# Kernel optimization log

Hardware: AMD Instinct MI355X
Metric: run time of the kernel (lower is better)

## Reference

```python
import math
import jax, jax.numpy as jnp
import numpy as np

NUM_HEADS = 8
K_CRITICAL = 0.05
K_SKIP = 0.10


def setup_inputs() -> dict:
    key = jax.random.key(0)
    ks = jax.random.split(key, 10)
    B, T, D = 1, 2048, 512
    s = 1.0 / math.sqrt(D)
    return {
        'x': jax.random.normal(ks[0], (B, T, D), jnp.float32),
        'wq': jax.random.normal(ks[1], (D, D), jnp.float32) * s,
        'bq': jax.random.normal(ks[2], (D,), jnp.float32) * s,
        'wk': jax.random.normal(ks[3], (D, D), jnp.float32) * s,
        'bk': jax.random.normal(ks[4], (D,), jnp.float32) * s,
        'wv': jax.random.normal(ks[5], (D, D), jnp.float32) * s,
        'bv': jax.random.normal(ks[6], (D,), jnp.float32) * s,
        'wo': jax.random.normal(ks[7], (D, D), jnp.float32) * s,
        'bo': jax.random.normal(ks[8], (D,), jnp.float32) * s,
    }


def _phi(t):
    # elu(t) + 1 -> positive feature map for linear attention
    return jax.nn.elu(t) + 1.0


def reference(x, wq, bq, wk, bk, wv, bv, wo, bo):
    B, T, D = x.shape
    H = NUM_HEADS
    hd = D // H

    # projections (torch nn.Linear: y = x @ W.T + b), split heads -> [B,H,T,hd]
    q = (x @ wq.T + bq).reshape(B, T, H, hd).transpose(0, 2, 1, 3)
    k = (x @ wk.T + bk).reshape(B, T, H, hd).transpose(0, 2, 1, 3)
    v = (x @ wv.T + bv).reshape(B, T, H, hd).transpose(0, 2, 1, 3)

    # full attention scores [B,H,T,T]
    scores = jnp.einsum('bhqd,bhkd->bhqk', q, k) / math.sqrt(hd)

    # per-query quantile thresholds (linear interpolation, like torch.quantile)
    crit_th = jnp.quantile(scores, 1.0 - K_CRITICAL, axis=-1, keepdims=True)
    skip_th = jnp.quantile(scores, K_SKIP, axis=-1, keepdims=True)
    crit_mask = scores > crit_th
    skip_mask = scores < skip_th
    marginal_mask = jnp.logical_not(crit_mask | skip_mask)

    # critical path: softmax over top-k_critical entries only
    crit_scores = jnp.where(crit_mask, scores, -jnp.inf)
    crit_attn = jax.nn.softmax(crit_scores, axis=-1)
    crit_attn = jnp.where(skip_mask, 0.0, crit_attn)
    crit_out = jnp.einsum('bhqk,bhkd->bhqd', crit_attn, v)

    # marginal path: causal (cumulative) linear attention
    q_f = _phi(q)
    k_f = _phi(k)
    kv_cum = jnp.cumsum(k_f[..., :, None] * v[..., None, :], axis=2)  # [B,H,T,hd,hd]
    k_cum = jnp.cumsum(k_f, axis=2)                                   # [B,H,T,hd]
    lin_num = jnp.einsum('bhtd,bhtde->bhte', q_f, kv_cum)             # [B,H,T,hd]
    lin_den = jnp.clip(jnp.sum(q_f * k_cum, axis=-1, keepdims=True), 1e-6, None)
    marginal_active = jnp.mean(marginal_mask.astype(scores.dtype), axis=-1, keepdims=True)
    lin_out = (lin_num / lin_den) * marginal_active

    out = (crit_out + lin_out).transpose(0, 2, 1, 3).reshape(B, T, D)
    out = out @ wo.T + bo  # dropout is identity in eval mode
    return out
```

## Files before the change

### kernel.cpp

```cpp
#include <hip/hip_runtime.h>
#include <math.h>

#define T_SEQ 2048
#define D_MODEL 512
#define H_HEADS 8
#define HD 64
#define NCH 32
#define CSZ 64
#define CAP 192

__device__ __forceinline__ unsigned f2k(float f) {
    unsigned u = __float_as_uint(f);
    return (u & 0x80000000u) ? ~u : (u | 0x80000000u);
}
__device__ __forceinline__ float k2f(unsigned k) {
    unsigned u = (k & 0x80000000u) ? (k & 0x7fffffffu) : ~k;
    return __uint_as_float(u);
}

__device__ __forceinline__ void locate_rank(unsigned rr, unsigned e0,
    const unsigned cc[4], int lane, unsigned& sel_bin, unsigned& sel_nb, unsigned& sel_cnt)
{
    unsigned e1 = e0 + cc[0], e2 = e1 + cc[1], e3 = e2 + cc[2];
    int bin = -1; unsigned nb = 0u, ct = 0u;
    if (rr >= e0 && rr < e1)              { bin = lane * 4 + 0; nb = e0; ct = cc[0]; }
    else if (rr >= e1 && rr < e2)         { bin = lane * 4 + 1; nb = e1; ct = cc[1]; }
    else if (rr >= e2 && rr < e3)         { bin = lane * 4 + 2; nb = e2; ct = cc[2]; }
    else if (rr >= e3 && rr < e3 + cc[3]) { bin = lane * 4 + 3; nb = e3; ct = cc[3]; }
    unsigned long long bal = __ballot(bin >= 0);
    int src = __ffsll((unsigned long long)bal) - 1;
    sel_bin = (unsigned)__shfl(bin, src);
    sel_nb  = (unsigned)__shfl((int)nb, src);
    sel_cnt = (unsigned)__shfl((int)ct, src);
}

__global__ __launch_bounds__(256) void proj_qkv_kernel(
    const float* __restrict__ x,
    const float* __restrict__ wq, const float* __restrict__ bq,
    const float* __restrict__ wk, const float* __restrict__ bk,
    const float* __restrict__ wv, const float* __restrict__ bv,
    float* __restrict__ qh, float* __restrict__ kh, float* __restrict__ vh,
    float* __restrict__ qf, float* __restrict__ kf)
{
    const int which = blockIdx.z;
    const float* W    = (which == 0) ? wq : (which == 1) ? wk : wv;
    const float* bias = (which == 0) ? bq : (which == 1) ? bk : bv;
    float* outh = (which == 0) ? qh : (which == 1) ? kh : vh;
    float* outf = (which == 0) ? qf : (which == 1) ? kf : nullptr;

    __shared__ float As[32][68];
    __shared__ float Bs[32][68];
    const int tid = threadIdx.x;
    const int m0 = blockIdx.x * 64;
    const int n0 = blockIdx.y * 64;
    const int rb = (tid >> 4) * 4;
    const int cb = (tid & 15) * 4;

    float acc[4][4] = {};
    for (int k0 = 0; k0 < D_MODEL; k0 += 32) {
        for (int l = 0; l < 2; ++l) {
            int p = tid + l * 256;
            int row = p >> 3;
            int c4 = (p & 7) * 4;
            float4 av = *(const float4*)(x + (size_t)(m0 + row) * D_MODEL + k0 + c4);
            As[c4 + 0][row] = av.x; As[c4 + 1][row] = av.y;
            As[c4 + 2][row] = av.z; As[c4 + 3][row] = av.w;
            float4 wv4 = *(const float4*)(W + (size_t)(n0 + row) * D_MODEL + k0 + c4);
            Bs[c4 + 0][row] = wv4.x; Bs[c4 + 1][row] = wv4.y;
            Bs[c4 + 2][row] = wv4.z; Bs[c4 + 3][row] = wv4.w;
        }
        __syncthreads();
        #pragma unroll
        for (int kk = 0; kk < 32; ++kk) {
            float4 ar = *(const float4*)&As[kk][rb];
            float4 br = *(const float4*)&Bs[kk][cb];
            float arr[4] = {ar.x, ar.y, ar.z, ar.w};
            float brr[4] = {br.x, br.y, br.z, br.w};
            #pragma unroll
            for (int i = 0; i < 4; ++i)
                #pragma unroll
                for (int j = 0; j < 4; ++j)
                    acc[i][j] = fmaf(arr[i], brr[j], acc[i][j]);
        }
        __syncthreads();
    }
    #pragma unroll
    for (int i = 0; i < 4; ++i) {
        int m = m0 + rb + i;
        #pragma unroll
        for (int j = 0; j < 4; ++j) {
            int n = n0 + cb + j;
            float v = acc[i][j] + bias[n];
            int h = n >> 6, d = n & 63;
            size_t idx = ((size_t)(h * T_SEQ) + m) * HD + d;
            outh[idx] = v;
            if (outf) outf[idx] = (v > 0.f) ? (v + 1.f) : __expf(v);
        }
    }
}

__global__ __launch_bounds__(256) void out_proj_kernel(
    const float* __restrict__ att, const float* __restrict__ wo,
    const float* __restrict__ bo, float* __restrict__ out)
{
    __shared__ float As[32][68];
    __shared__ float Bs[32][68];
    const int tid = threadIdx.x;
    const int m0 = blockIdx.x * 64;
    const int n0 = blockIdx.y * 64;
    const int rb = (tid >> 4) * 4;
    const int cb = (tid & 15) * 4;

    float acc[4][4] = {};
    for (int k0 = 0; k0 < D_MODEL; k0 += 32) {
        for (int l = 0; l < 2; ++l) {
            int p = tid + l * 256;
            int row = p >> 3;
            int c4 = (p & 7) * 4;
            float4 av = *(const float4*)(att + (size_t)(m0 + row) * D_MODEL + k0 + c4);
            As[c4 + 0][row] = av.x; As[c4 + 1][row] = av.y;
            As[c4 + 2][row] = av.z; As[c4 + 3][row] = av.w;
            float4 wv4 = *(const float4*)(wo + (size_t)(n0 + row) * D_MODEL + k0 + c4);
            Bs[c4 + 0][row] = wv4.x; Bs[c4 + 1][row] = wv4.y;
            Bs[c4 + 2][row] = wv4.z; Bs[c4 + 3][row] = wv4.w;
        }
        __syncthreads();
        #pragma unroll
        for (int kk = 0; kk < 32; ++kk) {
            float4 ar = *(const float4*)&As[kk][rb];
            float4 br = *(const float4*)&Bs[kk][cb];
            float arr[4] = {ar.x, ar.y, ar.z, ar.w};
            float brr[4] = {br.x, br.y, br.z, br.w};
            #pragma unroll
            for (int i = 0; i < 4; ++i)
                #pragma unroll
                for (int j = 0; j < 4; ++j)
                    acc[i][j] = fmaf(arr[i], brr[j], acc[i][j]);
        }
        __syncthreads();
    }
    #pragma unroll
    for (int i = 0; i < 4; ++i) {
        int m = m0 + rb + i;
        #pragma unroll
        for (int j = 0; j < 4; ++j) {
            int n = n0 + cb + j;
            out[(size_t)m * D_MODEL + n] = acc[i][j] + bo[n];
        }
    }
}

__global__ __launch_bounds__(256) void qk_gemm_kernel(
    const float* __restrict__ qh, const float* __restrict__ kh, float* __restrict__ S)
{
    __shared__ float As[64][132];
    __shared__ float Bs[64][68];
    const int tid = threadIdx.x;
    const int n0 = blockIdx.x * 64;
    const int m0 = blockIdx.y * 128;
    const int h  = blockIdx.z;
    const float* qb = qh + (size_t)h * T_SEQ * HD;
    const float* kb = kh + (size_t)h * T_SEQ * HD;

    #pragma unroll
    for (int l = 0; l < 8; ++l) {
        int p = tid + l * 256;
        int row = p >> 4, c4 = (p & 15) * 4;
        float4 a = *(const float4*)(qb + (size_t)(m0 + row) * HD + c4);
        As[c4 + 0][row] = a.x; As[c4 + 1][row] = a.y;
        As[c4 + 2][row] = a.z; As[c4 + 3][row] = a.w;
    }
    #pragma unroll
    for (int l = 0; l < 4; ++l) {
        int p = tid + l * 256;
        int row = p >> 4, c4 = (p & 15) * 4;
        float4 b = *(const float4*)(kb + (size_t)(n0 + row) * HD + c4);
        Bs[c4 + 0][row] = b.x; Bs[c4 + 1][row] = b.y;
        Bs[c4 + 2][row] = b.z; Bs[c4 + 3][row] = b.w;
    }
    __syncthreads();

    const int rb = (tid >> 4) * 8;
    const int cb = (tid & 15) * 4;
    float acc[8][4] = {};
    #pragma unroll 8
    for (int kk = 0; kk < HD; ++kk) {
        float4 a0 = *(const float4*)&As[kk][rb];
        float4 a1 = *(const float4*)&As[kk][rb + 4];
        float4 br = *(const float4*)&Bs[kk][cb];
        float arr[8] = {a0.x, a0.y, a0.z, a0.w, a1.x, a1.y, a1.z, a1.w};
        float brr[4] = {br.x, br.y, br.z, br.w};
        #pragma unroll
        for (int i = 0; i < 8; ++i)
            #pragma unroll
            for (int j = 0; j < 4; ++j)
                acc[i][j] = fmaf(arr[i], brr[j], acc[i][j]);
    }
    #pragma unroll
    for (int i = 0; i < 8; ++i) {
        float4 o;
        o.x = acc[i][0] * 0.125f; o.y = acc[i][1] * 0.125f;
        o.z = acc[i][2] * 0.125f; o.w = acc[i][3] * 0.125f;
        *(float4*)(S + ((size_t)h * T_SEQ + m0 + rb + i) * T_SEQ + n0 + cb) = o;
    }
}

__global__ __launch_bounds__(64, 8) void select_kernel(
    const float* __restrict__ S, const float* __restrict__ vh,
    float* __restrict__ att, float* __restrict__ marg)
{
    const int h = blockIdx.y;
    const int lane = threadIdx.x;
    const int t = blockIdx.x;
    __shared__ unsigned hists[2][256];

    const float* srow = S + ((size_t)h * T_SEQ + t) * T_SEQ;
    unsigned kr[32];
    unsigned mx = 0u;
    #pragma unroll
    for (int u = 0; u < 8; ++u) {
        float4 f = *(const float4*)(srow + (size_t)(lane + u * 64) * 4);
        kr[u * 4 + 0] = f2k(f.x); kr[u * 4 + 1] = f2k(f.y);
        kr[u * 4 + 2] = f2k(f.z); kr[u * 4 + 3] = f2k(f.w);
        mx = max(mx, max(max(kr[u * 4 + 0], kr[u * 4 + 1]), max(kr[u * 4 + 2], kr[u * 4 + 3])));
    }
    #pragma unroll
    for (int off = 32; off > 0; off >>= 1)
        mx = max(mx, (unsigned)__shfl_xor(mx, off));

    unsigned pfx0, pfx1, base0 = 0u, base1 = 0u, fct0 = 0u;
    bool res0 = false, res1 = false;
    unsigned rsh1 = 0u;

    {
        uint4 z4 = make_uint4(0u, 0u, 0u, 0u);
        uint4* hv = (uint4*)hists;
        hv[lane * 2 + 0] = z4; hv[lane * 2 + 1] = z4;
        #pragma unroll
        for (int u = 0; u < 32; ++u)
            atomicAdd(&hists[0][kr[u] >> 24], 1u);
        uint4 a = ((const uint4*)hists[0])[lane];
        unsigned cc[4] = {a.x, a.y, a.z, a.w};
        unsigned lsum = cc[0] + cc[1] + cc[2] + cc[3];
        unsigned incl = lsum;
        #pragma unroll
        for (int off = 1; off < 64; off <<= 1) {
            unsigned tv = __shfl_up(incl, off);
            if (lane >= off) incl += tv;
        }
        unsigned e0 = incl - lsum;
        unsigned bin, nb, ct;
        locate_rank(204u, e0, cc, lane, bin, nb, ct);
        pfx0 = bin; base0 = nb; fct0 = ct;
        if (ct == 1u) res0 = true;
        locate_rank(1944u, e0, cc, lane, bin, nb, ct);
        pfx1 = bin; base1 = nb;
        if (ct == 1u) { res1 = true; rsh1 = 24u; }
    }

    for (int p = 1; p < 4; ++p) {
        if (res0 && res1) break;
        const int sh = 24 - 8 * p;
        const bool a0 = !res0, a1 = !res1;
        const bool dup = a0 && a1 && (pfx0 == pfx1);
        uint4 z4 = make_uint4(0u, 0u, 0u, 0u);
        uint4* hv = (uint4*)hists;
        hv[lane * 2 + 0] = z4; hv[lane * 2 + 1] = z4;
        #pragma unroll
        for (int u = 0; u < 32; ++u) {
            unsigned k = kr[u];
            unsigned hi = k >> (sh + 8);
            unsigned bin = (k >> sh) & 255u;
            if (a0 && hi == pfx0) atomicAdd(&hists[0][bin], 1u);
            if (a1 && !dup && hi == pfx1) atomicAdd(&hists[1][bin], 1u);
        }
        unsigned cc0[4], e00 = 0u;
        if (a0 || dup) {
            uint4 a = ((const uint4*)hists[0])[lane];
            cc0[0] = a.x; cc0[1] = a.y; cc0[2] = a.z; cc0[3] = a.w;
            unsigned lsum = cc0[0] + cc0[1] + cc0[2] + cc0[3];
            unsigned incl = lsum;
            #pragma unroll
            for (int off = 1; off < 64; off <<= 1) {
                unsigned tv = __shfl_up(incl, off);
                if (lane >= off) incl += tv;
            }
            e00 = incl - lsum;
        }
        if (a0) {
            unsigned bin, nb, ct;
            locate_rank(204u - base0, e00, cc0, lane, bin, nb, ct);
            pfx0 = (pfx0 << 8) | bin; base0 += nb; fct0 = ct;
            if (ct == 1u && p < 3) res0 = true;
        }
        if (a1) {
            unsigned bin, nb, ct;
            if (dup) {
                locate_rank(1944u - base1, e00, cc0, lane, bin, nb, ct);
            } else {
                uint4 b = ((const uint4*)hists[1])[lane];
                unsigned cc1[4] = {b.x, b.y, b.z, b.w};
                unsigned lsum = cc1[0] + cc1[1] + cc1[2] + cc1[3];
                unsigned incl = lsum;
                #pragma unroll
                for (int off = 1; off < 64; off <<= 1) {
                    unsigned tv = __shfl_up(incl, off);
                    if (lane >= off) incl += tv;
                }
                unsigned e10 = incl - lsum;
                locate_rank(1944u - base1, e10, cc1, lane, bin, nb, ct);
            }
            pfx1 = (pfx1 << 8) | bin; base1 += nb;
            if (ct == 1u && p < 3) { res1 = true; rsh1 = (unsigned)sh; }
        }
    }

    const unsigned cle0 = base0 + fct0;
    const unsigned scnt = (cle0 > 205u) ? base0 : cle0;
    const float m = k2f(mx);

    float2* list = (float2*)hists;
    float z = 0.f;
    unsigned bcnt = 0;
    const unsigned long long pm = (lane == 0) ? 0ull : (~0ull >> (64 - lane));
    #pragma unroll
    for (int u8 = 0; u8 < 8; ++u8) {
        #pragma unroll
        for (int q = 0; q < 4; ++q) {
            unsigned k = kr[u8 * 4 + q];
            bool crit = (k >> rsh1) > pfx1;
            unsigned long long bal = __ballot(crit);
            if (crit) {
                float sv = k2f(k);
                float w = __expf(sv - m);
                z += w;
                unsigned pos = bcnt + (unsigned)__popcll(bal & pm);
                if (pos < CAP) {
                    unsigned j = (unsigned)(4 * lane + 256 * u8 + q);
                    list[pos] = make_float2(w, __uint_as_float(j));
                }
            }
            bcnt += (unsigned)__popcll(bal);
        }
    }
    #pragma unroll
    for (int off = 32; off > 0; off >>= 1)
        z += __shfl_xor(z, off);
    const float invz = (z > 0.f) ? (1.f / z) : 0.f;

    const float* vbl = vh + (size_t)h * T_SEQ * HD + lane;
    const int cnt = (int)min(bcnt, (unsigned)CAP);
    float av[8];
    #pragma unroll
    for (int q = 0; q < 8; ++q) av[q] = 0.f;
    int i = 0;
    for (; i + 8 <= cnt; i += 8) {
        float2 e[8];
        #pragma unroll
        for (int q = 0; q < 8; ++q) e[q] = list[i + q];
        float vv[8];
        #pragma unroll
        for (int q = 0; q < 8; ++q)
            vv[q] = vbl[(size_t)__float_as_uint(e[q].y) * HD];
        #pragma unroll
        for (int q = 0; q < 8; ++q)
            av[q] = fmaf(e[q].x, vv[q], av[q]);
    }
    for (; i < cnt; ++i) {
        float2 e = list[i];
        av[0] = fmaf(e.x, vbl[(size_t)__float_as_uint(e.y) * HD], av[0]);
    }
    float acc = ((av[0] + av[1]) + (av[2] + av[3])) + ((av[4] + av[5]) + (av[6] + av[7]));
    att[(size_t)t * D_MODEL + h * HD + lane] = acc * invz;
    if (lane == 0) {
        unsigned mc = (unsigned)T_SEQ - bcnt - scnt;
        marg[(size_t)h * T_SEQ + t] = (float)mc * (1.f / (float)T_SEQ);
    }
}

__global__ __launch_bounds__(256) void chunk_sums_kernel(
    const float* __restrict__ kf, const float* __restrict__ vh,
    float* __restrict__ Ac, float* __restrict__ bc)
{
    const int c = blockIdx.x, h = blockIdx.y;
    const int tid = threadIdx.x;
    __shared__ float kfl[CSZ][HD];
    __shared__ float vl[CSZ][HD];
    const size_t base = ((size_t)h * T_SEQ + c * CSZ) * HD;

    for (int l = 0; l < 4; ++l) {
        int p = tid + l * 256;
        int row = p >> 4, c4 = (p & 15) * 4;
        *(float4*)&kfl[row][c4] = *(const float4*)(kf + base + (size_t)row * HD + c4);
        *(float4*)&vl[row][c4]  = *(const float4*)(vh + base + (size_t)row * HD + c4);
    }
    __syncthreads();

    const int d = tid >> 2, e0 = (tid & 3) * 16;
    float acc[16] = {};
    for (int u = 0; u < CSZ; ++u) {
        float a = kfl[u][d];
        #pragma unroll
        for (int i = 0; i < 16; ++i) acc[i] = fmaf(a, vl[u][e0 + i], acc[i]);
    }
    float* Adst = Ac + (((size_t)(h * NCH + c) * HD + d) * HD + e0);
    #pragma unroll
    for (int i = 0; i < 16; ++i) Adst[i] = acc[i];

    if (tid < HD) {
        float sum = 0.f;
        for (int u = 0; u < CSZ; ++u) sum += kfl[u][tid];
        bc[(size_t)(h * NCH + c) * HD + tid] = sum;
    }
}

__global__ __launch_bounds__(256) void lin_combine_kernel(
    const float* __restrict__ qf, const float* __restrict__ kf, const float* __restrict__ vh,
    const float* __restrict__ Ac, const float* __restrict__ bc,
    const float* __restrict__ marg, float* __restrict__ att)
{
    const int c = blockIdx.x, h = blockIdx.y;
    const int tid = threadIdx.x;
    __shared__ float Qs[CSZ][65];
    __shared__ float Ks[CSZ][65];
    __shared__ float P[CSZ][66];
    __shared__ float svv[HD];
    __shared__ float coef[CSZ];

    const size_t base = ((size_t)h * T_SEQ + c * CSZ) * HD;
    for (int l = 0; l < 4; ++l) {
        int p = tid + l * 256;
        int row = p >> 4, c4 = (p & 15) * 4;
        *(float4*)&Qs[row][c4] = *(const float4*)(qf + base + (size_t)row * HD + c4);
        *(float4*)&Ks[row][c4] = *(const float4*)(kf + base + (size_t)row * HD + c4);
    }

    float4 sA[4];
    #pragma unroll
    for (int l = 0; l < 4; ++l) sA[l] = make_float4(0.f, 0.f, 0.f, 0.f);
    float sb = 0.f;
    {
        const float* Abase = Ac + (size_t)(h * NCH) * 4096;
        for (int cc = 0; cc < c; ++cc) {
            const float* a = Abase + (size_t)cc * 4096;
            #pragma unroll
            for (int l = 0; l < 4; ++l) {
                float4 v = *(const float4*)(a + 4 * (tid + l * 256));
                sA[l].x += v.x; sA[l].y += v.y; sA[l].z += v.z; sA[l].w += v.w;
            }
            if (tid < HD) sb += bc[(size_t)(h * NCH + cc) * HD + tid];
        }
    }
    __syncthreads();

    {
        const int tq = tid >> 2, u0 = (tid & 3) * 16;
        float pr[16];
        #pragma unroll
        for (int i = 0; i < 16; ++i) pr[i] = 0.f;
        for (int d = 0; d < HD; ++d) {
            float qv = Qs[tq][d];
            #pragma unroll
            for (int i = 0; i < 16; ++i) pr[i] = fmaf(qv, Ks[u0 + i][d], pr[i]);
        }
        #pragma unroll
        for (int i = 0; i < 16; ++i) P[tq][u0 + i] = (u0 + i <= tq) ? pr[i] : 0.f;
    }
    __syncthreads();

    #pragma unroll
    for (int l = 0; l < 4; ++l) {
        int p = tid + l * 256;
        int row = p >> 4, c4 = (p & 15) * 4;
        *(float4*)&Ks[row][c4] = sA[l];
    }
    if (tid < HD) svv[tid] = sb;
    if (tid < CSZ) {
        const int tq = tid;
        float den = 0.f;
        for (int d = 0; d < HD; ++d) den += Qs[tq][d] * svv[d];
        for (int u = 0; u <= tq; ++u) den += P[tq][u];
        den = fmaxf(den, 1e-6f);
        coef[tq] = marg[(size_t)h * T_SEQ + c * CSZ + tq] / den;
    }
    __syncthreads();

    {
        const int tq = tid >> 2, e0 = (tid & 3) * 16;
        float acc[16];
        #pragma unroll
        for (int i = 0; i < 16; ++i) acc[i] = 0.f;
        for (int d = 0; d < HD; ++d) {
            float qv = Qs[tq][d];
            #pragma unroll
            for (int i = 0; i < 16; ++i) acc[i] = fmaf(qv, Ks[d][e0 + i], acc[i]);
        }
        const float* vb = vh + base;
        for (int u = 0; u <= tq; ++u) {
            float pv = P[tq][u];
            #pragma unroll
            for (int i = 0; i < 16; ++i) acc[i] = fmaf(pv, vb[(size_t)u * HD + e0 + i], acc[i]);
        }
        const float cf = coef[tq];
        float* dst = att + (size_t)(c * CSZ + tq) * D_MODEL + h * HD + e0;
        #pragma unroll
        for (int i = 0; i < 16; ++i) dst[i] += acc[i] * cf;
    }
}

extern "C" void kernel_launch(void* const* d_in, const int* in_sizes, int n_in,
                              void* d_out, int out_size, void* d_ws, size_t ws_size,
                              hipStream_t stream)
{
    const float* x  = (const float*)d_in[0];
    const float* wq = (const float*)d_in[1];
    const float* bq = (const float*)d_in[2];
    const float* wk = (const float*)d_in[3];
    const float* bk = (const float*)d_in[4];
    const float* wv = (const float*)d_in[5];
    const float* bv = (const float*)d_in[6];
    const float* wo = (const float*)d_in[7];
    const float* bo = (const float*)d_in[8];
    float* out = (float*)d_out;

    float* ws = (float*)d_ws;
    const size_t NTD = (size_t)T_SEQ * D_MODEL;
    const size_t NSS = (size_t)H_HEADS * T_SEQ * T_SEQ;
    float* S    = ws;
    float* qh   = S + NSS;
    float* kh   = qh + NTD;
    float* vh   = kh + NTD;
    float* qf   = vh + NTD;
    float* kf   = qf + NTD;
    float* att  = kf + NTD;
    float* Ac   = att + NTD;
    float* bc   = Ac + NTD;
    float* marg = bc + 16384;

    dim3 b256(256);
    proj_qkv_kernel<<<dim3(32, 8, 3), b256, 0, stream>>>(x, wq, bq, wk, bk, wv, bv,
                                                         qh, kh, vh, qf, kf);
    chunk_sums_kernel<<<dim3(NCH, H_HEADS), b256, 0, stream>>>(kf, vh, Ac, bc);
    qk_gemm_kernel<<<dim3(32, 16, 8), b256, 0, stream>>>(qh, kh, S);
    select_kernel<<<dim3(T_SEQ, H_HEADS), dim3(64), 0, stream>>>(S, vh, att, marg);
    lin_combine_kernel<<<dim3(NCH, H_HEADS), b256, 0, stream>>>(qf, kf, vh, Ac, bc, marg, att);
    out_proj_kernel<<<dim3(32, 8), b256, 0, stream>>>(att, wo, bo, out);
}
```

Before: 286.8 us.

## Replace LDS radix-histogram selection with ballot-based bitwise rank search

The per-row quantile selection used multi-pass 8-bit radix histograms in shared memory with atomics, prefix scans and rank location. It is replaced by a 32-step bitwise binary search over the order-preserving keys, counting candidates with wave ballots and popcounts for both thresholds at once. This removes the LDS atomics and scans, but always runs 32 passes of 64 ballots each, where the histogram path often finished early. Shared memory now holds only the critical list.

```diff
diff --git a/kernel.cpp b/kernel.cpp
--- a/kernel.cpp
+++ b/kernel.cpp
@@ -16,22 +16,6 @@
 __device__ __forceinline__ float k2f(unsigned k) {
     unsigned u = (k & 0x80000000u) ? (k & 0x7fffffffu) : ~k;
     return __uint_as_float(u);
-}
-
-__device__ __forceinline__ void locate_rank(unsigned rr, unsigned e0,
-    const unsigned cc[4], int lane, unsigned& sel_bin, unsigned& sel_nb, unsigned& sel_cnt)
-{
-    unsigned e1 = e0 + cc[0], e2 = e1 + cc[1], e3 = e2 + cc[2];
-    int bin = -1; unsigned nb = 0u, ct = 0u;
-    if (rr >= e0 && rr < e1)              { bin = lane * 4 + 0; nb = e0; ct = cc[0]; }
-    else if (rr >= e1 && rr < e2)         { bin = lane * 4 + 1; nb = e1; ct = cc[1]; }
-    else if (rr >= e2 && rr < e3)         { bin = lane * 4 + 2; nb = e2; ct = cc[2]; }
-    else if (rr >= e3 && rr < e3 + cc[3]) { bin = lane * 4 + 3; nb = e3; ct = cc[3]; }
-    unsigned long long bal = __ballot(bin >= 0);
-    int src = __ffsll((unsigned long long)bal) - 1;
-    sel_bin = (unsigned)__shfl(bin, src);
-    sel_nb  = (unsigned)__shfl((int)nb, src);
-    sel_cnt = (unsigned)__shfl((int)ct, src);
 }
 
 __global__ __launch_bounds__(256) void proj_qkv_kernel(
@@ -212,7 +196,7 @@
     const int h = blockIdx.y;
     const int lane = threadIdx.x;
     const int t = blockIdx.x;
-    __shared__ unsigned hists[2][256];
+    __shared__ float2 list[CAP];
 
     const float* srow = S + ((size_t)h * T_SEQ + t) * T_SEQ;
     unsigned kr[32];
@@ -228,98 +212,31 @@
     for (int off = 32; off > 0; off >>= 1)
         mx = max(mx, (unsigned)__shfl_xor(mx, off));
 
-    unsigned pfx0, pfx1, base0 = 0u, base1 = 0u, fct0 = 0u;
-    bool res0 = false, res1 = false;
-    unsigned rsh1 = 0u;
-
-    {
-        uint4 z4 = make_uint4(0u, 0u, 0u, 0u);
-        uint4* hv = (uint4*)hists;
-        hv[lane * 2 + 0] = z4; hv[lane * 2 + 1] = z4;
-        #pragma unroll
-        for (int u = 0; u < 32; ++u)
-            atomicAdd(&hists[0][kr[u] >> 24], 1u);
-        uint4 a = ((const uint4*)hists[0])[lane];
-        unsigned cc[4] = {a.x, a.y, a.z, a.w};
-        unsigned lsum = cc[0] + cc[1] + cc[2] + cc[3];
-        unsigned incl = lsum;
-        #pragma unroll
-        for (int off = 1; off < 64; off <<= 1) {
-            unsigned tv = __shfl_up(incl, off);
-            if (lane >= off) incl += tv;
-        }
-        unsigned e0 = incl - lsum;
-        unsigned bin, nb, ct;
-        locate_rank(204u, e0, cc, lane, bin, nb, ct);
-        pfx0 = bin; base0 = nb; fct0 = ct;
-        if (ct == 1u) res0 = true;
-        locate_rank(1944u, e0, cc, lane, bin, nb, ct);
-        pfx1 = bin; base1 = nb;
-        if (ct == 1u) { res1 = true; rsh1 = 24u; }
-    }
-
-    for (int p = 1; p < 4; ++p) {
-        if (res0 && res1) break;
-        const int sh = 24 - 8 * p;
-        const bool a0 = !res0, a1 = !res1;
-        const bool dup = a0 && a1 && (pfx0 == pfx1);
-        uint4 z4 = make_uint4(0u, 0u, 0u, 0u);
-        uint4* hv = (uint4*)hists;
-        hv[lane * 2 + 0] = z4; hv[lane * 2 + 1] = z4;
+    unsigned kth0 = 0u, kth1 = 0u;
+    for (int b = 31; b >= 0; --b) {
+        const unsigned bit = 1u << b;
+        const unsigned t0 = kth0 | bit, t1 = kth1 | bit;
+        unsigned c0 = 0u, c1 = 0u;
         #pragma unroll
         for (int u = 0; u < 32; ++u) {
-            unsigned k = kr[u];
-            unsigned hi = k >> (sh + 8);
-            unsigned bin = (k >> sh) & 255u;
-            if (a0 && hi == pfx0) atomicAdd(&hists[0][bin], 1u);
-            if (a1 && !dup && hi == pfx1) atomicAdd(&hists[1][bin], 1u);
-        }
-        unsigned cc0[4], e00 = 0u;
-        if (a0 || dup) {
-            uint4 a = ((const uint4*)hists[0])[lane];
-            cc0[0] = a.x; cc0[1] = a.y; cc0[2] = a.z; cc0[3] = a.w;
-            unsigned lsum = cc0[0] + cc0[1] + cc0[2] + cc0[3];
-            unsigned incl = lsum;
-            #pragma unroll
-            for (int off = 1; off < 64; off <<= 1) {
-                unsigned tv = __shfl_up(incl, off);
-                if (lane >= off) incl += tv;
-            }
-            e00 = incl - lsum;
-        }
-        if (a0) {
-            unsigned bin, nb, ct;
-            locate_rank(204u - base0, e00, cc0, lane, bin, nb, ct);
-            pfx0 = (pfx0 << 8) | bin; base0 += nb; fct0 = ct;
-            if (ct == 1u && p < 3) res0 = true;
-        }
-        if (a1) {
-            unsigned bin, nb, ct;
-            if (dup) {
-                locate_rank(1944u - base1, e00, cc0, lane, bin, nb, ct);
-            } else {
-                uint4 b = ((const uint4*)hists[1])[lane];
-                unsigned cc1[4] = {b.x, b.y, b.z, b.w};
-                unsigned lsum = cc1[0] + cc1[1] + cc1[2] + cc1[3];
-                unsigned incl = lsum;
-                #pragma unroll
-                for (int off = 1; off < 64; off <<= 1) {
-                    unsigned tv = __shfl_up(incl, off);
-                    if (lane >= off) incl += tv;
-                }
-                unsigned e10 = incl - lsum;
-                locate_rank(1944u - base1, e10, cc1, lane, bin, nb, ct);
-            }
-            pfx1 = (pfx1 << 8) | bin; base1 += nb;
-            if (ct == 1u && p < 3) { res1 = true; rsh1 = (unsigned)sh; }
-        }
-    }
-
-    const unsigned cle0 = base0 + fct0;
+            c0 += (unsigned)__popcll(__ballot(kr[u] >= t0));
+            c1 += (unsigned)__popcll(__ballot(kr[u] >= t1));
+        }
+        if (c0 >= (unsigned)(T_SEQ - 204))  kth0 = t0;
+        if (c1 >= (unsigned)(T_SEQ - 1944)) kth1 = t1;
+    }
+
+    unsigned cge0 = 0u, cgt0 = 0u;
+    #pragma unroll
+    for (int u = 0; u < 32; ++u) {
+        cge0 += (unsigned)__popcll(__ballot(kr[u] >= kth0));
+        cgt0 += (unsigned)__popcll(__ballot(kr[u] > kth0));
+    }
+    const unsigned base0 = (unsigned)T_SEQ - cge0;
+    const unsigned cle0  = (unsigned)T_SEQ - cgt0;
     const unsigned scnt = (cle0 > 205u) ? base0 : cle0;
     const float m = k2f(mx);
 
-    float2* list = (float2*)hists;
     float z = 0.f;
     unsigned bcnt = 0;
     const unsigned long long pm = (lane == 0) ? 0ull : (~0ull >> (64 - lane));
@@ -328,7 +245,7 @@
         #pragma unroll
         for (int q = 0; q < 4; ++q) {
             unsigned k = kr[u8 * 4 + q];
-            bool crit = (k >> rsh1) > pfx1;
+            bool crit = k > kth1;
             unsigned long long bal = __ballot(crit);
             if (crit) {
                 float sv = k2f(k);
```

Measured after the change: 345.0 us. 20.3% more time.
